# Kernel tuning notes

Hardware: AMD Instinct MI355X
Metric: run time of the kernel (lower is better)

Reference implementation:

```python
import jax, jax.numpy as jnp
import numpy as np

S, B, E = 512, 512, 768

def setup_inputs() -> dict:
    key = jax.random.key(0)
    k1, k2, k3 = jax.random.split(key, 3)
    inputs = jax.random.normal(k1, (S, B, E), dtype=jnp.float32)
    rotation_params = jax.random.normal(k2, (E, E), dtype=jnp.float32)
    entangle_params = jax.random.normal(k3, (E, E), dtype=jnp.float32)
    return {"inputs": inputs, "rotation_params": rotation_params, "entangle_params": entangle_params}

def reference(inputs, rotation_params, entangle_params):
    seq_len, batch, embed_dim = inputs.shape
    # Q/K projections: (S,B,E) @ (E,E) -> (S,B,E)
    q = jnp.einsum('sbe,ef->sbf', inputs, rotation_params.reshape(embed_dim, -1))
    k = jnp.einsum('sbe,ef->sbf', inputs, entangle_params.reshape(embed_dim, -1))
    v = inputs
    # Faithful to the torch code: matmul batches over seq_len, so attention
    # mixes across the BATCH axis -> scores shape (S, B, B).
    scale = 1.0 / jnp.sqrt(jnp.float32(embed_dim))
    scores = jax.nn.softmax(jnp.einsum('sbe,sce->sbc', q, k) * scale, axis=-1)
    return jnp.einsum('sbc,sce->sbe', scores, v)
```

## Files before the change

kernel.cpp:

```cpp
#include <hip/hip_runtime.h>
#include <math.h>

typedef unsigned short ushort_t;
typedef __attribute__((ext_vector_type(8))) short bf16x8;
typedef __attribute__((ext_vector_type(4))) float f32x4;

#define SD 512
#define BD 512
#define ED 768
#define SCALE 0.03608439182435161f

__device__ __forceinline__ ushort_t f2bf(float f) {
  unsigned u = __float_as_uint(f);
  return (ushort_t)((u + 0x7FFFu + ((u >> 16) & 1u)) >> 16);
}
__device__ __forceinline__ float bf2f(ushort_t h) {
  return __uint_as_float(((unsigned)h) << 16);
}

struct MMP {
  const float* Af;
  const ushort_t* Ahi; const ushort_t* Alo;
  long aLd, aZ;
  const float* Bf;
  const ushort_t* Bhi; const ushort_t* Blo;
  long bLd, bZ;
  float* Cf; float cScale;
  ushort_t* Chi; ushort_t* Clo;
  long cLd, cZ;
  int zMode;
  int K;
};

template <int AM, int BM, int EPI, bool TRIPLE>
__global__ __launch_bounds__(256) void mm(MMP P)
{
  __shared__ ushort_t lds[16384];
  ushort_t* Ah = lds;
  ushort_t* Al = lds + 4096;
  ushort_t* Bh = lds + 8192;
  ushort_t* Bl = lds + 12288;

  const int tid = threadIdx.x;
  const int z = blockIdx.z;
  int bx = blockIdx.x, by = blockIdx.y;
  if (gridDim.z == 1) {
    int nwg = gridDim.x * gridDim.y;
    if ((nwg & 7) == 0) {
      int id = by * gridDim.x + bx;
      int q = nwg >> 3;
      int wid = (id & 7) * q + (id >> 3);
      bx = wid % gridDim.x;
      by = wid / gridDim.x;
    }
  }
  const int m0 = by * 128, n0 = bx * 128;

  const int lane = tid & 63;
  const int wave = tid >> 6;
  const int wm = (wave >> 1) * 64, wn = (wave & 1) * 64;
  const int lr = lane & 15, g = lane >> 4;

  f32x4 acc[4][4];
  #pragma unroll
  for (int i = 0; i < 4; ++i)
    #pragma unroll
    for (int j = 0; j < 4; ++j) {
      f32x4 zv = {0.f, 0.f, 0.f, 0.f};
      acc[i][j] = zv;
    }

  for (int k0 = 0; k0 < P.K; k0 += 32) {
    if constexpr (AM == 0) {
      const float* A = P.Af + (long)z * P.aZ;
      #pragma unroll
      for (int rep = 0; rep < 4; ++rep) {
        int idx = tid + rep * 256;
        int row = idx >> 3, q = idx & 7;
        float4 v = *(const float4*)(A + (long)(m0 + row) * P.aLd + k0 + q * 4);
        int off = row * 32 + (((q >> 1) ^ ((row >> 1) & 3)) << 3) + ((q & 1) << 2);
        ushort_t hh[4], ll[4];
        hh[0] = f2bf(v.x); ll[0] = f2bf(v.x - bf2f(hh[0]));
        hh[1] = f2bf(v.y); ll[1] = f2bf(v.y - bf2f(hh[1]));
        hh[2] = f2bf(v.z); ll[2] = f2bf(v.z - bf2f(hh[2]));
        hh[3] = f2bf(v.w); ll[3] = f2bf(v.w - bf2f(hh[3]));
        *(uint2*)(Ah + off) = *(uint2*)hh;
        *(uint2*)(Al + off) = *(uint2*)ll;
      }
    } else {
      const ushort_t* As = P.Ahi + (long)z * P.aZ;
      #pragma unroll
      for (int rep = 0; rep < 2; ++rep) {
        int idx = tid + rep * 256;
        int row = idx >> 2, h8 = idx & 3;
        int off = row * 32 + ((h8 ^ ((row >> 1) & 3)) << 3);
        long gsrc = (long)(m0 + row) * P.aLd + k0 + h8 * 8;
        *(uint4*)(Ah + off) = *(const uint4*)(As + gsrc);
        if constexpr (AM == 1) {
          const ushort_t* Als = P.Alo + (long)z * P.aZ;
          *(uint4*)(Al + off) = *(const uint4*)(Als + gsrc);
        }
      }
    }
    if constexpr (BM == 0) {
      const float* B = P.Bf + (long)z * P.bZ;
      #pragma unroll
      for (int rep = 0; rep < 4; ++rep) {
        int idx = tid + rep * 256;
        int row = idx >> 3, q = idx & 7;
        float4 v = *(const float4*)(B + (long)(n0 + row) * P.bLd + k0 + q * 4);
        int off = row * 32 + (((q >> 1) ^ ((row >> 1) & 3)) << 3) + ((q & 1) << 2);
        ushort_t hh[4], ll[4];
        hh[0] = f2bf(v.x); ll[0] = f2bf(v.x - bf2f(hh[0]));
        hh[1] = f2bf(v.y); ll[1] = f2bf(v.y - bf2f(hh[1]));
        hh[2] = f2bf(v.z); ll[2] = f2bf(v.z - bf2f(hh[2]));
        hh[3] = f2bf(v.w); ll[3] = f2bf(v.w - bf2f(hh[3]));
        *(uint2*)(Bh + off) = *(uint2*)hh;
        *(uint2*)(Bl + off) = *(uint2*)ll;
      }
    } else {
      const ushort_t* Bs = P.Bhi + (long)z * P.bZ;
      #pragma unroll
      for (int rep = 0; rep < 2; ++rep) {
        int idx = tid + rep * 256;
        int row = idx >> 2, h8 = idx & 3;
        int off = row * 32 + ((h8 ^ ((row >> 1) & 3)) << 3);
        long gsrc = (long)(n0 + row) * P.bLd + k0 + h8 * 8;
        *(uint4*)(Bh + off) = *(const uint4*)(Bs + gsrc);
        if constexpr (BM == 1) {
          const ushort_t* Bls = P.Blo + (long)z * P.bZ;
          *(uint4*)(Bl + off) = *(const uint4*)(Bls + gsrc);
        }
      }
    }
    __syncthreads();

    bf16x8 ar[4], br[4];
    #pragma unroll
    for (int i = 0; i < 4; ++i) {
      int row = wm + i * 16 + lr;
      ar[i] = *(const bf16x8*)(Ah + row * 32 + ((g ^ ((row >> 1) & 3)) << 3));
    }
    #pragma unroll
    for (int j = 0; j < 4; ++j) {
      int row = wn + j * 16 + lr;
      br[j] = *(const bf16x8*)(Bh + row * 32 + ((g ^ ((row >> 1) & 3)) << 3));
    }
    #pragma unroll
    for (int i = 0; i < 4; ++i)
      #pragma unroll
      for (int j = 0; j < 4; ++j)
        acc[i][j] = __builtin_amdgcn_mfma_f32_16x16x32_bf16(ar[i], br[j], acc[i][j], 0, 0, 0);

    if constexpr (TRIPLE) {
      #pragma unroll
      for (int j = 0; j < 4; ++j) {
        int row = wn + j * 16 + lr;
        bf16x8 blv = *(const bf16x8*)(Bl + row * 32 + ((g ^ ((row >> 1) & 3)) << 3));
        #pragma unroll
        for (int i = 0; i < 4; ++i)
          acc[i][j] = __builtin_amdgcn_mfma_f32_16x16x32_bf16(ar[i], blv, acc[i][j], 0, 0, 0);
      }
      #pragma unroll
      for (int i = 0; i < 4; ++i) {
        int row = wm + i * 16 + lr;
        bf16x8 alv = *(const bf16x8*)(Al + row * 32 + ((g ^ ((row >> 1) & 3)) << 3));
        #pragma unroll
        for (int j = 0; j < 4; ++j)
          acc[i][j] = __builtin_amdgcn_mfma_f32_16x16x32_bf16(alv, br[j], acc[i][j], 0, 0, 0);
      }
    }
    __syncthreads();
  }

  #pragma unroll
  for (int i = 0; i < 4; ++i) {
    #pragma unroll
    for (int j = 0; j < 4; ++j) {
      int colG = n0 + wn + j * 16 + lr;
      #pragma unroll
      for (int r = 0; r < 4; ++r) {
        int rowG = m0 + wm + i * 16 + g * 4 + r;
        float v = acc[i][j][r];
        if constexpr (EPI == 0) {
          P.Cf[(long)z * P.cZ + (long)rowG * P.cLd + colG] = v * P.cScale;
        } else {
          ushort_t hi = f2bf(v);
          ushort_t lo = f2bf(v - bf2f(hi));
          long off;
          if (P.zMode) off = (long)(rowG >> 9) * 786432 + (long)(rowG & 511) * 768 + colG;
          else         off = (long)rowG * P.cLd + colG;
          P.Chi[off] = hi;
          P.Clo[off] = lo;
        }
      }
    }
  }
}

__global__ __launch_bounds__(256) void softmax_rows(const float* __restrict__ S,
                                                    ushort_t* __restrict__ Pm)
{
  const int z = blockIdx.y;
  const int row = blockIdx.x * 4 + (threadIdx.x >> 6);
  const int lane = threadIdx.x & 63;
  const float* Sr = S + (long)z * 262144 + (long)row * 512 + lane * 8;
  float x[8];
  *(float4*)&x[0] = *(const float4*)(Sr);
  *(float4*)&x[4] = *(const float4*)(Sr + 4);
  float m = x[0];
  #pragma unroll
  for (int i = 1; i < 8; ++i) m = fmaxf(m, x[i]);
  #pragma unroll
  for (int off = 32; off >= 1; off >>= 1) m = fmaxf(m, __shfl_xor(m, off, 64));
  float e[8], sum = 0.f;
  #pragma unroll
  for (int i = 0; i < 8; ++i) { e[i] = __expf(x[i] - m); sum += e[i]; }
  #pragma unroll
  for (int off = 32; off >= 1; off >>= 1) sum += __shfl_xor(sum, off, 64);
  float inv = 1.0f / sum;
  ushort_t h[8];
  #pragma unroll
  for (int i = 0; i < 8; ++i) h[i] = f2bf(e[i] * inv);
  *(uint4*)(Pm + (long)z * 262144 + (long)row * 512 + lane * 8) = *(uint4*)h;
}

__global__ __launch_bounds__(256) void transpose_split(const float* __restrict__ X,
                                                       ushort_t* __restrict__ Xt, int s0)
{
  const int si = blockIdx.z;
  const long s = s0 + si;
  const int b0 = blockIdx.x * 64, e0 = blockIdx.y * 64;
  __shared__ float tile[64][65];
  const int t = threadIdx.x;
  const int bloc = t >> 4, eq = t & 15;
  #pragma unroll
  for (int r = 0; r < 4; ++r) {
    int b = bloc + r * 16;
    float4 v = *(const float4*)(X + (s * 512 + b0 + b) * 768 + e0 + eq * 4);
    tile[b][eq * 4 + 0] = v.x; tile[b][eq * 4 + 1] = v.y;
    tile[b][eq * 4 + 2] = v.z; tile[b][eq * 4 + 3] = v.w;
  }
  __syncthreads();
  const int e = t & 63, bq = t >> 6;
  ushort_t tmp[16];
  #pragma unroll
  for (int i = 0; i < 16; ++i) tmp[i] = f2bf(tile[bq * 16 + i][e]);
  ushort_t* dst = Xt + (long)si * 393216 + (long)(e0 + e) * 512 + b0 + bq * 16;
  *(uint4*)(dst)     = *(uint4*)&tmp[0];
  *(uint4*)(dst + 8) = *(uint4*)&tmp[8];
}

extern "C" void kernel_launch(void* const* d_in, const int* in_sizes, int n_in,
                              void* d_out, int out_size, void* d_ws, size_t ws_size,
                              hipStream_t stream) {
  const float* X = (const float*)d_in[0];
  const float* R = (const float*)d_in[1];
  const float* W = (const float*)d_in[2];
  float* out = (float*)d_out;
  char* ws = (char*)d_ws;

  ushort_t* Hhi = (ushort_t*)ws;
  ushort_t* Hlo = Hhi + 768 * 768;
  const size_t hBytes = 2ull * 768 * 768 * 2;
  const size_t perS   = 262144ull * 4 + 262144ull * 2 + 393216ull * 2;
  long SCI = 1;
  if (ws_size > hBytes + perS) SCI = (long)((ws_size - hBytes) / perS);
  if (SCI < 1) SCI = 1;
  if (SCI > 512) SCI = 512;
  float*    scores = (float*)(ws + hBytes);
  ushort_t* Pm     = (ushort_t*)(ws + hBytes + (size_t)SCI * 1048576ull);
  ushort_t* Xt     = (ushort_t*)((char*)Pm + (size_t)SCI * 524288ull);

  {
    MMP p{};
    p.Af = W;  p.aLd = 768; p.aZ = 0;
    p.Bf = R;  p.bLd = 768; p.bZ = 0;
    p.Chi = Hhi; p.Clo = Hlo; p.cLd = 768; p.zMode = 0;
    p.K = 768;
    mm<0, 0, 1, true><<<dim3(6, 6, 1), 256, 0, stream>>>(p);
  }
  {
    MMP p{};
    p.Af = X; p.aLd = 768; p.aZ = 0;
    p.Bhi = Hhi; p.Blo = Hlo; p.bLd = 768; p.bZ = 0;
    p.Chi = (ushort_t*)d_out; p.Clo = (ushort_t*)d_out + 393216; p.zMode = 1;
    p.K = 768;
    mm<0, 1, 1, true><<<dim3(6, 2048, 1), 256, 0, stream>>>(p);
  }

  for (long s0 = 0; s0 < 512; s0 += SCI) {
    int cur = (int)((512 - s0 < SCI) ? (512 - s0) : SCI);
    {
      MMP p{};
      p.Ahi = (const ushort_t*)d_out + s0 * 786432;
      p.Alo = p.Ahi + 393216;
      p.aLd = 768; p.aZ = 786432;
      p.Bf = X + s0 * 393216; p.bLd = 768; p.bZ = 393216;
      p.Cf = scores; p.cLd = 512; p.cZ = 262144; p.cScale = SCALE;
      p.K = 768;
      mm<1, 0, 0, true><<<dim3(4, 4, cur), 256, 0, stream>>>(p);
    }
    softmax_rows<<<dim3(128, cur), 256, 0, stream>>>(scores, Pm);
    transpose_split<<<dim3(8, 12, cur), 256, 0, stream>>>(X, Xt, (int)s0);
    {
      MMP p{};
      p.Ahi = Pm; p.aLd = 512; p.aZ = 262144;
      p.Bhi = Xt; p.bLd = 512; p.bZ = 393216;
      p.Cf = out + s0 * 393216; p.cLd = 768; p.cZ = 393216; p.cScale = 1.0f;
      p.K = 512;
      mm<2, 2, 0, false><<<dim3(6, 4, cur), 256, 0, stream>>>(p);
    }
  }
}
```

Measured before the change: 3.167 ms.

## Fuse score matmul with softmax and pre-split X once per chunk

Adds a fused kernel that computes the QK^T-style scores with split-bf16 MFMA and applies the row softmax in registers, writing bf16 probabilities directly. This removes the fp32 scores buffer round trip and the separate softmax launch. X is now split into hi/lo bf16 once per chunk in the prep kernel, which also does the transpose, so the split is shared by the projection and the score kernels. The projection moves inside the chunk loop and reads the pre-split X. Each fused block holds a full 512-wide row of the score tile, which raises LDS use and cuts the number of blocks per chunk.

```diff
diff --git a/kernel.cpp b/kernel.cpp
--- a/kernel.cpp
+++ b/kernel.cpp
@@ -5,9 +5,6 @@
 typedef __attribute__((ext_vector_type(8))) short bf16x8;
 typedef __attribute__((ext_vector_type(4))) float f32x4;
 
-#define SD 512
-#define BD 512
-#define ED 768
 #define SCALE 0.03608439182435161f
 
 __device__ __forceinline__ ushort_t f2bf(float f) {
@@ -21,7 +18,7 @@
 struct MMP {
   const float* Af;
   const ushort_t* Ahi; const ushort_t* Alo;
-  long aLd, aZ;
+  long aLd, aZ; int aSplitS;
   const float* Bf;
   const ushort_t* Bhi; const ushort_t* Blo;
   long bLd, bZ;
@@ -87,19 +84,33 @@
         *(uint2*)(Ah + off) = *(uint2*)hh;
         *(uint2*)(Al + off) = *(uint2*)ll;
       }
-    } else {
-      const ushort_t* As = P.Ahi + (long)z * P.aZ;
+    } else if constexpr (AM == 1) {
       #pragma unroll
       for (int rep = 0; rep < 2; ++rep) {
         int idx = tid + rep * 256;
         int row = idx >> 2, h8 = idx & 3;
         int off = row * 32 + ((h8 ^ ((row >> 1) & 3)) << 3);
-        long gsrc = (long)(m0 + row) * P.aLd + k0 + h8 * 8;
-        *(uint4*)(Ah + off) = *(const uint4*)(As + gsrc);
-        if constexpr (AM == 1) {
-          const ushort_t* Als = P.Alo + (long)z * P.aZ;
-          *(uint4*)(Al + off) = *(const uint4*)(Als + gsrc);
+        int rg = m0 + row;
+        const ushort_t *As, *Als;
+        if (P.aSplitS) {
+          long base = (long)(rg >> 9) * 786432 + (long)(rg & 511) * 768 + k0 + h8 * 8;
+          As = P.Ahi + base; Als = P.Ahi + base + 393216;
+        } else {
+          long base = (long)rg * P.aLd + k0 + h8 * 8;
+          As = P.Ahi + (long)z * P.aZ + base;
+          Als = P.Alo + (long)z * P.aZ + base;
         }
+        *(uint4*)(Ah + off) = *(const uint4*)As;
+        *(uint4*)(Al + off) = *(const uint4*)Als;
+      }
+    } else {
+      const ushort_t* As = P.Ahi + (long)z * P.aZ;
+      #pragma unroll
+      for (int rep = 0; rep < 2; ++rep) {
+        int idx = tid + rep * 256;
+        int row = idx >> 2, h8 = idx & 3;
+        int off = row * 32 + ((h8 ^ ((row >> 1) & 3)) << 3);
+        *(uint4*)(Ah + off) = *(const uint4*)(As + (long)(m0 + row) * P.aLd + k0 + h8 * 8);
       }
     }
     if constexpr (BM == 0) {
@@ -198,35 +209,142 @@
   }
 }
 
-__global__ __launch_bounds__(256) void softmax_rows(const float* __restrict__ S,
-                                                    ushort_t* __restrict__ Pm)
+__global__ __launch_bounds__(512) void fsc(const ushort_t* __restrict__ Zb,
+                                           const ushort_t* __restrict__ Xs,
+                                           ushort_t* __restrict__ Pm)
 {
+  __shared__ ushort_t lds[36864];
+  __shared__ float redf[64][12];
+  __shared__ float reds[64][12];
+  ushort_t* Ah = lds;
+  ushort_t* Al = lds + 2048;
+  ushort_t* Bh = lds + 4096;
+  ushort_t* Bl = lds + 20480;
+
   const int z = blockIdx.y;
-  const int row = blockIdx.x * 4 + (threadIdx.x >> 6);
-  const int lane = threadIdx.x & 63;
-  const float* Sr = S + (long)z * 262144 + (long)row * 512 + lane * 8;
-  float x[8];
-  *(float4*)&x[0] = *(const float4*)(Sr);
-  *(float4*)&x[4] = *(const float4*)(Sr + 4);
-  float m = x[0];
-  #pragma unroll
-  for (int i = 1; i < 8; ++i) m = fmaxf(m, x[i]);
-  #pragma unroll
-  for (int off = 32; off >= 1; off >>= 1) m = fmaxf(m, __shfl_xor(m, off, 64));
-  float e[8], sum = 0.f;
-  #pragma unroll
-  for (int i = 0; i < 8; ++i) { e[i] = __expf(x[i] - m); sum += e[i]; }
-  #pragma unroll
-  for (int off = 32; off >= 1; off >>= 1) sum += __shfl_xor(sum, off, 64);
-  float inv = 1.0f / sum;
-  ushort_t h[8];
-  #pragma unroll
-  for (int i = 0; i < 8; ++i) h[i] = f2bf(e[i] * inv);
-  *(uint4*)(Pm + (long)z * 262144 + (long)row * 512 + lane * 8) = *(uint4*)h;
-}
-
-__global__ __launch_bounds__(256) void transpose_split(const float* __restrict__ X,
-                                                       ushort_t* __restrict__ Xt, int s0)
+  const ushort_t* Az = Zb + (long)z * 786432;
+  const ushort_t* Bz = Xs + (long)z * 786432;
+  const int m0 = blockIdx.x * 64;
+
+  const int tid = threadIdx.x;
+  const int lane = tid & 63;
+  const int wave = tid >> 6;
+  const int wn = wave * 64;
+  const int lr = lane & 15, g = lane >> 4;
+
+  f32x4 acc[4][4];
+  #pragma unroll
+  for (int i = 0; i < 4; ++i)
+    #pragma unroll
+    for (int j = 0; j < 4; ++j) {
+      f32x4 zv = {0.f, 0.f, 0.f, 0.f};
+      acc[i][j] = zv;
+    }
+
+  for (int k0 = 0; k0 < 768; k0 += 32) {
+    {
+      int e = tid & 255;
+      int row = e >> 2, h8 = e & 3;
+      int off = row * 32 + ((h8 ^ ((row >> 1) & 3)) << 3);
+      long src = (long)(m0 + row) * 768 + k0 + h8 * 8;
+      if (tid < 256) *(uint4*)(Ah + off) = *(const uint4*)(Az + src);
+      else           *(uint4*)(Al + off) = *(const uint4*)(Az + 393216 + src);
+    }
+    #pragma unroll
+    for (int rep = 0; rep < 8; ++rep) {
+      int e = (tid + rep * 512) & 2047;
+      int row = e >> 2, h8 = e & 3;
+      int off = row * 32 + ((h8 ^ ((row >> 1) & 3)) << 3);
+      long src = (long)row * 768 + k0 + h8 * 8;
+      if (rep < 4) *(uint4*)(Bh + off) = *(const uint4*)(Bz + src);
+      else         *(uint4*)(Bl + off) = *(const uint4*)(Bz + 393216 + src);
+    }
+    __syncthreads();
+
+    bf16x8 arh[4], arl[4];
+    #pragma unroll
+    for (int i = 0; i < 4; ++i) {
+      int row = i * 16 + lr;
+      int off = row * 32 + ((g ^ ((row >> 1) & 3)) << 3);
+      arh[i] = *(const bf16x8*)(Ah + off);
+      arl[i] = *(const bf16x8*)(Al + off);
+    }
+    #pragma unroll
+    for (int j = 0; j < 4; ++j) {
+      int row = wn + j * 16 + lr;
+      int off = row * 32 + ((g ^ ((row >> 1) & 3)) << 3);
+      bf16x8 bh = *(const bf16x8*)(Bh + off);
+      bf16x8 bl = *(const bf16x8*)(Bl + off);
+      #pragma unroll
+      for (int i = 0; i < 4; ++i) {
+        acc[i][j] = __builtin_amdgcn_mfma_f32_16x16x32_bf16(arh[i], bh, acc[i][j], 0, 0, 0);
+        acc[i][j] = __builtin_amdgcn_mfma_f32_16x16x32_bf16(arh[i], bl, acc[i][j], 0, 0, 0);
+        acc[i][j] = __builtin_amdgcn_mfma_f32_16x16x32_bf16(arl[i], bh, acc[i][j], 0, 0, 0);
+      }
+    }
+    __syncthreads();
+  }
+
+  float mr[4][4];
+  #pragma unroll
+  for (int i = 0; i < 4; ++i)
+    #pragma unroll
+    for (int r = 0; r < 4; ++r) {
+      float mx = -3.0e38f;
+      #pragma unroll
+      for (int j = 0; j < 4; ++j) {
+        acc[i][j][r] *= SCALE;
+        mx = fmaxf(mx, acc[i][j][r]);
+      }
+      #pragma unroll
+      for (int off = 8; off >= 1; off >>= 1) mx = fmaxf(mx, __shfl_xor(mx, off, 64));
+      if (lr == 0) redf[i * 16 + g * 4 + r][wave] = mx;
+    }
+  __syncthreads();
+  #pragma unroll
+  for (int i = 0; i < 4; ++i)
+    #pragma unroll
+    for (int r = 0; r < 4; ++r) {
+      int row = i * 16 + g * 4 + r;
+      float4 a = *(const float4*)&redf[row][0];
+      float4 b = *(const float4*)&redf[row][4];
+      mr[i][r] = fmaxf(fmaxf(fmaxf(a.x, a.y), fmaxf(a.z, a.w)),
+                       fmaxf(fmaxf(b.x, b.y), fmaxf(b.z, b.w)));
+    }
+  #pragma unroll
+  for (int i = 0; i < 4; ++i)
+    #pragma unroll
+    for (int r = 0; r < 4; ++r) {
+      float s = 0.f;
+      #pragma unroll
+      for (int j = 0; j < 4; ++j) {
+        float e = __expf(acc[i][j][r] - mr[i][r]);
+        acc[i][j][r] = e;
+        s += e;
+      }
+      #pragma unroll
+      for (int off = 8; off >= 1; off >>= 1) s += __shfl_xor(s, off, 64);
+      if (lr == 0) reds[i * 16 + g * 4 + r][wave] = s;
+    }
+  __syncthreads();
+  ushort_t* Pz = Pm + (long)z * 262144 + (long)m0 * 512;
+  #pragma unroll
+  for (int i = 0; i < 4; ++i)
+    #pragma unroll
+    for (int r = 0; r < 4; ++r) {
+      int row = i * 16 + g * 4 + r;
+      float4 a = *(const float4*)&reds[row][0];
+      float4 b = *(const float4*)&reds[row][4];
+      float inv = 1.0f / (a.x + a.y + a.z + a.w + b.x + b.y + b.z + b.w);
+      #pragma unroll
+      for (int j = 0; j < 4; ++j)
+        Pz[(long)row * 512 + wn + j * 16 + lr] = f2bf(acc[i][j][r] * inv);
+    }
+}
+
+__global__ __launch_bounds__(256) void prep(const float* __restrict__ X,
+                                            ushort_t* __restrict__ Xsp,
+                                            ushort_t* __restrict__ Xt, int s0)
 {
   const int si = blockIdx.z;
   const long s = s0 + si;
@@ -234,12 +352,21 @@
   __shared__ float tile[64][65];
   const int t = threadIdx.x;
   const int bloc = t >> 4, eq = t & 15;
+  ushort_t* Xh = Xsp + (long)si * 786432;
   #pragma unroll
   for (int r = 0; r < 4; ++r) {
     int b = bloc + r * 16;
     float4 v = *(const float4*)(X + (s * 512 + b0 + b) * 768 + e0 + eq * 4);
     tile[b][eq * 4 + 0] = v.x; tile[b][eq * 4 + 1] = v.y;
     tile[b][eq * 4 + 2] = v.z; tile[b][eq * 4 + 3] = v.w;
+    ushort_t hh[4], ll[4];
+    hh[0] = f2bf(v.x); ll[0] = f2bf(v.x - bf2f(hh[0]));
+    hh[1] = f2bf(v.y); ll[1] = f2bf(v.y - bf2f(hh[1]));
+    hh[2] = f2bf(v.z); ll[2] = f2bf(v.z - bf2f(hh[2]));
+    hh[3] = f2bf(v.w); ll[3] = f2bf(v.w - bf2f(hh[3]));
+    long dst = (long)(b0 + b) * 768 + e0 + eq * 4;
+    *(uint2*)(Xh + dst)          = *(uint2*)hh;
+    *(uint2*)(Xh + 393216 + dst) = *(uint2*)ll;
   }
   __syncthreads();
   const int e = t & 63, bq = t >> 6;
@@ -262,15 +389,15 @@
 
   ushort_t* Hhi = (ushort_t*)ws;
   ushort_t* Hlo = Hhi + 768 * 768;
-  const size_t hBytes = 2ull * 768 * 768 * 2;
-  const size_t perS   = 262144ull * 4 + 262144ull * 2 + 393216ull * 2;
+  const size_t hB   = 2ull * 768 * 768 * 2;
+  const size_t perS = 786432ull * 2 + 393216ull * 2 + 262144ull * 2;
   long SCI = 1;
-  if (ws_size > hBytes + perS) SCI = (long)((ws_size - hBytes) / perS);
+  if (ws_size > hB + perS) SCI = (long)((ws_size - hB) / perS);
   if (SCI < 1) SCI = 1;
   if (SCI > 512) SCI = 512;
-  float*    scores = (float*)(ws + hBytes);
-  ushort_t* Pm     = (ushort_t*)(ws + hBytes + (size_t)SCI * 1048576ull);
-  ushort_t* Xt     = (ushort_t*)((char*)Pm + (size_t)SCI * 524288ull);
+  ushort_t* Xsp = (ushort_t*)(ws + hB);
+  ushort_t* Xt  = Xsp + (long)SCI * 786432;
+  ushort_t* Pm  = Xt + (long)SCI * 393216;
 
   {
     MMP p{};
@@ -280,36 +407,32 @@
     p.K = 768;
     mm<0, 0, 1, true><<<dim3(6, 6, 1), 256, 0, stream>>>(p);
   }
-  {
-    MMP p{};
-    p.Af = X; p.aLd = 768; p.aZ = 0;
-    p.Bhi = Hhi; p.Blo = Hlo; p.bLd = 768; p.bZ = 0;
-    p.Chi = (ushort_t*)d_out; p.Clo = (ushort_t*)d_out + 393216; p.zMode = 1;
-    p.K = 768;
-    mm<0, 1, 1, true><<<dim3(6, 2048, 1), 256, 0, stream>>>(p);
-  }
 
   for (long s0 = 0; s0 < 512; s0 += SCI) {
     int cur = (int)((512 - s0 < SCI) ? (512 - s0) : SCI);
+
+    prep<<<dim3(8, 12, cur), 256, 0, stream>>>(X, Xsp, Xt, (int)s0);
+
     {
       MMP p{};
-      p.Ahi = (const ushort_t*)d_out + s0 * 786432;
-      p.Alo = p.Ahi + 393216;
-      p.aLd = 768; p.aZ = 786432;
-      p.Bf = X + s0 * 393216; p.bLd = 768; p.bZ = 393216;
-      p.Cf = scores; p.cLd = 512; p.cZ = 262144; p.cScale = SCALE;
+      p.Ahi = Xsp; p.aSplitS = 1; p.aLd = 768; p.aZ = 0;
+      p.Bhi = Hhi; p.Blo = Hlo; p.bLd = 768; p.bZ = 0;
+      p.Chi = (ushort_t*)d_out + s0 * 786432;
+      p.Clo = p.Chi + 393216;
+      p.zMode = 1;
       p.K = 768;
-      mm<1, 0, 0, true><<<dim3(4, 4, cur), 256, 0, stream>>>(p);
-    }
-    softmax_rows<<<dim3(128, cur), 256, 0, stream>>>(scores, Pm);
-    transpose_split<<<dim3(8, 12, cur), 256, 0, stream>>>(X, Xt, (int)s0);
+      mm<1, 1, 1, true><<<dim3(6, 4 * cur, 1), 256, 0, stream>>>(p);
+    }
+
+    fsc<<<dim3(8, cur), 512, 0, stream>>>((const ushort_t*)d_out + s0 * 786432, Xsp, Pm);
+
     {
-      MMP p{};
-      p.Ahi = Pm; p.aLd = 512; p.aZ = 262144;
-      p.Bhi = Xt; p.bLd = 512; p.bZ = 393216;
-      p.Cf = out + s0 * 393216; p.cLd = 768; p.cZ = 393216; p.cScale = 1.0f;
-      p.K = 512;
-      mm<2, 2, 0, false><<<dim3(6, 4, cur), 256, 0, stream>>>(p);
-    }
-  }
-}
+      MMP q{};
+      q.Ahi = Pm; q.aLd = 512; q.aZ = 262144; q.aSplitS = 0;
+      q.Bhi = Xt; q.bLd = 512; q.bZ = 393216;
+      q.Cf = out + s0 * 393216; q.cLd = 768; q.cZ = 393216; q.cScale = 1.0f;
+      q.K = 512;
+      mm<2, 2, 0, false><<<dim3(6, 4, cur), 256, 0, stream>>>(q);
+    }
+  }
+}
```

Measured after the change: 3.917 ms. 23.7% more time.
